# Performance work log

Measured on AMD Instinct MI355X. Metric: run time of the kernel, lower is better.

## Reference

```python
import jax, jax.numpy as jnp
import numpy as np

B, C, H = 16, 256, 32          # batch, in_channels(=out_channels), image_size
HEADS, HS = 8, 32              # heads = out_channels // head_size
D = HEADS * HS                 # head_dim = 256
N = H * H                      # tokens = 1024
EPS = 1e-5


def _rel_indices(h, w):
    # Faithful port of RelativeAttention2d.get_indices
    y = np.arange(h)
    x = np.arange(w)
    y1, x1, y2, x2 = np.meshgrid(y, x, y, x, indexing='ij')
    idx = (y1 - y2 + h - 1) * (2 * w - 1) + (x1 - x2 + w - 1)
    return jnp.asarray(idx.reshape(-1), dtype=jnp.int32)  # [N*N]


def setup_inputs() -> dict:
    key = jax.random.key(0)
    ks = jax.random.split(key, 10)
    s = 0.02
    return {
        'x': jax.random.normal(ks[0], (B, C, H, H), jnp.float32),
        'ln_g': jnp.ones((C,), jnp.float32),
        'ln_b': jnp.zeros((C,), jnp.float32),
        'wq': jax.random.normal(ks[1], (D, C), jnp.float32) * s,
        'bq': jnp.zeros((D,), jnp.float32),
        'wk': jax.random.normal(ks[2], (D, C), jnp.float32) * s,
        'bk': jnp.zeros((D,), jnp.float32),
        'wv': jax.random.normal(ks[3], (D, C), jnp.float32) * s,
        'bv': jnp.zeros((D,), jnp.float32),
        'wo': jax.random.normal(ks[4], (C, D), jnp.float32) * s,
        'bo': jnp.zeros((C,), jnp.float32),
        'rel_bias': jax.random.normal(ks[5], (HEADS, (2 * H - 1) * (2 * H - 1)), jnp.float32),
        'rel_idx': _rel_indices(H, H),
    }


def reference(x, ln_g, ln_b, wq, bq, wk, bk, wv, bv, wo, bo, rel_bias, rel_idx):
    b = x.shape[0]
    # norm(): LayerNorm over channel axis (dim 1 after the double transpose)
    mu = jnp.mean(x, axis=1, keepdims=True)
    var = jnp.mean((x - mu) ** 2, axis=1, keepdims=True)
    xn = (x - mu) / jnp.sqrt(var + EPS)
    xn = xn * ln_g[None, :, None, None] + ln_b[None, :, None, None]
    # reshape_for_linear: raw reshape [b, C, H, W] -> [b, N, C] (as in torch)
    xr = xn.reshape(b, N, C)
    # projections, then raw view(b, heads, head_size, -1) as in torch
    q = (xr @ wq.T + bq).reshape(b, HEADS, HS, N)
    k = (xr @ wk.T + bk).reshape(b, HEADS, HS, N)
    v = (xr @ wv.T + bv).reshape(b, HEADS, HS, N)
    # dots = k^T q / sqrt(head_dim)   [b, heads, N, N]
    dots = jnp.einsum('bhdn,bhdm->bhnm', k, q) / np.float32(np.sqrt(D))
    # gathered relative position bias  [heads, N, N]
    bias = rel_bias[:, rel_idx].reshape(HEADS, N, N)
    attn = jax.nn.softmax(dots + bias[None], axis=-2)  # non-standard softmax dim
    # out = v @ attn  [b, heads, head_size, N]
    out = jnp.einsum('bhdn,bhnm->bhdm', v, attn)
    out = out.reshape(b, H, H, D)  # raw view as in torch
    out = out @ wo.T + bo          # to_output linear (dropout is identity in eval)
    out = out.reshape(b, C, H, H)  # raw view back to [b, out_channels, H, W]
    return x + out
```

## Files before the change

### kernel.cpp

```cpp
#include <hip/hip_runtime.h>
#include <cstdint>

#define PERB 262144
#define LOG2EF 1.4426950408889634f
#define C1F 0.09016844005556022f

typedef __attribute__((ext_vector_type(8))) short bf16x8;
typedef __attribute__((ext_vector_type(4))) float f32x4;
typedef unsigned short ushort_t;

__device__ __forceinline__ uint16_t f2bf(float f) {
    uint32_t u = __float_as_uint(f);
    u += 0x7fff + ((u >> 16) & 1);
    return (uint16_t)(u >> 16);
}

__device__ __forceinline__ void glds16(const void* g, void* l) {
    __builtin_amdgcn_global_load_lds(
        (const __attribute__((address_space(1))) void*)g,
        (__attribute__((address_space(3))) void*)l, 16, 0, 0);
}

__global__ __launch_bounds__(256) void prep_kernel(
    const float* __restrict__ x, const float* __restrict__ gam,
    const float* __restrict__ bet, ushort_t* __restrict__ X,
    const float* __restrict__ wq, const float* __restrict__ wk,
    const float* __restrict__ wv, const float* __restrict__ wo,
    ushort_t* __restrict__ oq, ushort_t* __restrict__ ok,
    ushort_t* __restrict__ ov, ushort_t* __restrict__ oo,
    const float* __restrict__ rb, float* __restrict__ rb2)
{
    const int blk = blockIdx.x;
    const int tid = threadIdx.x;
    if (blk < 256) {
        const int which = blk >> 6;
        const int idx = ((blk & 63) * 256 + tid) * 4;
        const float* src = which == 0 ? wq : which == 1 ? wk : which == 2 ? wv : wo;
        ushort_t* dst    = which == 0 ? oq : which == 1 ? ok : which == 2 ? ov : oo;
        const float4 v = *(const float4*)&src[idx];
        uint2 p;
        p.x = (uint32_t)f2bf(v.x) | ((uint32_t)f2bf(v.y) << 16);
        p.y = (uint32_t)f2bf(v.z) | ((uint32_t)f2bf(v.w) << 16);
        *(uint2*)&dst[idx] = p;
        return;
    }
    if (blk >= 512) {
        const int h = blk - 512;
        const float* s = rb + h * 3969;
        float* d = rb2 + h * 3969;
        for (int i = tid; i < 3969; i += 256) d[i] = s[i] * LOG2EF;
        return;
    }
    const int lb  = blk - 256;
    const int b   = lb >> 4;
    const int sp0 = (lb & 15) << 6;
    const int v   = tid & 15;
    const int cg  = tid >> 4;
    const int sp  = sp0 + v * 4;
    const float* xb = x + (size_t)b * PERB + sp;

    float4 vals[16];
    float4 s4 = {0.f, 0.f, 0.f, 0.f}, q4 = {0.f, 0.f, 0.f, 0.f};
#pragma unroll
    for (int i = 0; i < 16; ++i) {
        const float4 t = *(const float4*)&xb[(size_t)(cg * 16 + i) * 1024];
        vals[i] = t;
        s4.x += t.x; s4.y += t.y; s4.z += t.z; s4.w += t.w;
        q4.x += t.x * t.x; q4.y += t.y * t.y; q4.z += t.z * t.z; q4.w += t.w * t.w;
    }
    __shared__ float red[2][16][64];
    __shared__ float mr[2][64];
    *(float4*)&red[0][cg][v * 4] = s4;
    *(float4*)&red[1][cg][v * 4] = q4;
    __syncthreads();
    if (tid < 64) {
        float ts = 0.f, tq = 0.f;
#pragma unroll
        for (int g = 0; g < 16; ++g) { ts += red[0][g][tid]; tq += red[1][g][tid]; }
        const float mean = ts * (1.f / 256.f);
        const float var  = tq * (1.f / 256.f) - mean * mean;
        mr[0][tid] = mean;
        mr[1][tid] = rsqrtf(var + 1e-5f);
    }
    __syncthreads();
    const float4 mean4 = *(const float4*)&mr[0][v * 4];
    const float4 rstd4 = *(const float4*)&mr[1][v * 4];

    ushort_t* Xb = X + (size_t)b * PERB + sp;
#pragma unroll
    for (int i = 0; i < 16; ++i) {
        const int c = cg * 16 + i;
        const float g = gam[c], be = bet[c];
        const float4 t = vals[i];
        const float y0 = (t.x - mean4.x) * rstd4.x * g + be;
        const float y1 = (t.y - mean4.y) * rstd4.y * g + be;
        const float y2 = (t.z - mean4.z) * rstd4.z * g + be;
        const float y3 = (t.w - mean4.w) * rstd4.w * g + be;
        uint2 p;
        p.x = (uint32_t)f2bf(y0) | ((uint32_t)f2bf(y1) << 16);
        p.y = (uint32_t)f2bf(y2) | ((uint32_t)f2bf(y3) << 16);
        *(uint2*)&Xb[(size_t)c * 1024] = p;
    }
}

__device__ __forceinline__ void qkv_stage(
    ushort_t* Sb, const ushort_t* __restrict__ X,
    const ushort_t* __restrict__ wq, const ushort_t* __restrict__ wk,
    const ushort_t* __restrict__ wv,
    int m0, int n0, int k0, int w, int lane)
{
    const int rsub = lane >> 3;
    const int u    = lane & 7;
    const int koct = u ^ rsub;
#pragma unroll
    for (int i = 0; i < 2; ++i) {
        const int rg  = w * 2 + i;
        const int row = rg * 8 + rsub;
        const int go  = k0 + koct * 8;
        ushort_t* db = Sb + rg * 512;
        glds16(&X [(size_t)(m0 + row) * 256 + go], db);
        glds16(&wq[(size_t)(n0 + row) * 256 + go], db + 4096);
        glds16(&wk[(size_t)(n0 + row) * 256 + go], db + 8192);
        glds16(&wv[(size_t)(n0 + row) * 256 + go], db + 12288);
    }
}

__device__ __forceinline__ void qkv_compute(
    const ushort_t* Sb, int w, int c, int quad, f32x4 acc[3][4])
{
#pragma unroll
    for (int ks = 0; ks < 2; ++ks) {
        const int kq = ks * 4 + quad;
        const int uo = (kq ^ (c & 7)) * 8;
        bf16x8 af[4];
#pragma unroll
        for (int msub = 0; msub < 4; ++msub)
            af[msub] = *(const bf16x8*)&Sb[(msub * 16 + c) * 64 + uo];
        bf16x8 bw[3];
#pragma unroll
        for (int o3 = 0; o3 < 3; ++o3)
            bw[o3] = *(const bf16x8*)&Sb[(o3 + 1) * 4096 + (w * 16 + c) * 64 + uo];
#pragma unroll
        for (int o3 = 0; o3 < 3; ++o3)
#pragma unroll
            for (int msub = 0; msub < 4; ++msub)
                acc[o3][msub] = __builtin_amdgcn_mfma_f32_16x16x32_bf16(
                    bw[o3], af[msub], acc[o3][msub], 0, 0, 0);
    }
}

__global__ __launch_bounds__(256) void qkv_kernel(
    const ushort_t* __restrict__ X,
    const ushort_t* __restrict__ wq, const float* __restrict__ bq,
    const ushort_t* __restrict__ wk, const float* __restrict__ bk,
    const ushort_t* __restrict__ wv, const float* __restrict__ bv,
    ushort_t* __restrict__ Q, ushort_t* __restrict__ K, ushort_t* __restrict__ V)
{
    __shared__ __align__(16) ushort_t SB0[4][4096];
    __shared__ __align__(16) ushort_t SB1[4][4096];

    const int blk = blockIdx.x;
    const int m0  = (blk >> 2) << 6;
    const int n0  = (blk & 3) << 6;
    const int tid = threadIdx.x;
    const int w    = tid >> 6;
    const int lane = tid & 63;
    const int quad = lane >> 4;
    const int c    = lane & 15;

    f32x4 acc[3][4];
#pragma unroll
    for (int o3 = 0; o3 < 3; ++o3)
#pragma unroll
        for (int i = 0; i < 4; ++i) acc[o3][i] = (f32x4){0.f, 0.f, 0.f, 0.f};

    qkv_stage(&SB0[0][0], X, wq, wk, wv, m0, n0, 0, w, lane);
    __syncthreads();
#pragma unroll
    for (int kc = 0; kc < 4; ++kc) {
        if (kc < 3) {
            if ((kc & 1) == 0)
                qkv_stage(&SB1[0][0], X, wq, wk, wv, m0, n0, (kc + 1) << 6, w, lane);
            else
                qkv_stage(&SB0[0][0], X, wq, wk, wv, m0, n0, (kc + 1) << 6, w, lane);
        }
        if ((kc & 1) == 0) qkv_compute(&SB0[0][0], w, c, quad, acc);
        else               qkv_compute(&SB1[0][0], w, c, quad, acc);
        __syncthreads();
    }

    const int n = n0 + w * 16 + quad * 4;
    const float4 bq4 = *(const float4*)&bq[n];
    const float4 bk4 = *(const float4*)&bk[n];
    const float4 bv4 = *(const float4*)&bv[n];
    ushort_t* outs[3] = {Q, K, V};
    const float4 bias[3] = {bq4, bk4, bv4};
#pragma unroll
    for (int msub = 0; msub < 4; ++msub) {
        const size_t m = (size_t)(m0 + msub * 16 + c);
#pragma unroll
        for (int o3 = 0; o3 < 3; ++o3) {
            const f32x4 a = acc[o3][msub];
            uint2 p;
            p.x = (uint32_t)f2bf(a[0] + bias[o3].x) | ((uint32_t)f2bf(a[1] + bias[o3].y) << 16);
            p.y = (uint32_t)f2bf(a[2] + bias[o3].z) | ((uint32_t)f2bf(a[3] + bias[o3].w) << 16);
            *(uint2*)&outs[o3][m * 256 + n] = p;
        }
    }
}

__global__ __launch_bounds__(256, 4) void attn_kernel(
    const ushort_t* __restrict__ Q, const ushort_t* __restrict__ K,
    const ushort_t* __restrict__ V, const float* __restrict__ relb2,
    ushort_t* __restrict__ O)
{
    __shared__ __align__(16) unsigned char smem[32768];
    char* Pb = (char*)smem;
    char* Kl = (char*)(smem + 16384);
    char* Vl = (char*)(smem + 24576);

    const int blk = blockIdx.x;
    const int bh  = blk & 127;
    const int mt  = blk >> 7;
    const int b   = bh >> 3;
    const int h   = bh & 7;
    const int m0  = mt << 7;
    const int tid = threadIdx.x;
    const int w    = tid >> 6;
    const int lane = tid & 63;
    const int quad = lane >> 4;
    const int c    = lane & 15;

    const size_t base = (size_t)b * PERB + (size_t)h * 32768;
    const ushort_t* Qg = Q + base;
    const ushort_t* Kg = K + base;
    const ushort_t* Vg = V + base;
    const float* rbh = relb2 + h * 3969;

    const int knn = tid & 63, ksg = tid >> 6;
    const int vs  = tid >> 3, vng = tid & 7;
    const int kWr = ksg * 1024 + knn * 16;
    const int vWr = vs * 128 + ((vng ^ (vs & 7)) << 4);
    const int c7  = c & 7;

    uint32_t kpre[8]; bf16x8 vpre;
#pragma unroll
    for (int j = 0; j < 8; ++j) kpre[j] = Kg[(size_t)(ksg * 8 + j) * 1024 + knn];
    vpre = *(const bf16x8*)&Vg[(size_t)vs * 1024 + vng * 8];

    {
        const int mm = tid & 127;
        const int sg = tid >> 7;
        union { bf16x8 v; uint16_t u[8]; } g0, g1;
#pragma unroll
        for (int j = 0; j < 8; ++j)
            g0.u[j] = Qg[(size_t)(sg * 16 + j) * 1024 + m0 + mm];
#pragma unroll
        for (int j = 0; j < 8; ++j)
            g1.u[j] = Qg[(size_t)(sg * 16 + 8 + j) * 1024 + m0 + mm];
        *(bf16x8*)(Pb + (sg * 2 + 0) * 2048 + mm * 16) = g0.v;
        *(bf16x8*)(Pb + (sg * 2 + 1) * 2048 + mm * 16) = g1.v;
    }
    {
        uint4 kp;
        kp.x = kpre[0] | (kpre[1] << 16);
        kp.y = kpre[2] | (kpre[3] << 16);
        kp.z = kpre[4] | (kpre[5] << 16);
        kp.w = kpre[6] | (kpre[7] << 16);
        *(uint4*)(Kl + kWr) = kp;
        *(bf16x8*)(Vl + vWr) = vpre;
    }
    __syncthreads();

    bf16x8 qfrag[2];
#pragma unroll
    for (int mi = 0; mi < 2; ++mi)
        qfrag[mi] = *(const bf16x8*)(Pb + quad * 2048 + (((w * 2 + mi) * 16 + c)) * 16);
    __syncthreads();

    int moff[2];
#pragma unroll
    for (int mi = 0; mi < 2; ++mi) {
        const int m = m0 + (w * 2 + mi) * 16 + c;
        moff[mi] = 1984 - (m >> 5) * 63 - (m & 31);
    }
    const int rowb0 = ((w * 2 + 0) * 16 + c) * 128;
    const int rowb1 = ((w * 2 + 1) * 16 + c) * 128;

    f32x4 oacc[2][2], dacc[2];
#pragma unroll
    for (int i = 0; i < 2; ++i) {
        dacc[i] = (f32x4){0.f, 0.f, 0.f, 0.f};
#pragma unroll
        for (int j = 0; j < 2; ++j) oacc[i][j] = (f32x4){0.f, 0.f, 0.f, 0.f};
    }
    bf16x8 onesf;
#pragma unroll
    for (int j = 0; j < 8; ++j) onesf[j] = (short)0x3F80;

#pragma unroll
    for (int j = 0; j < 8; ++j) kpre[j] = Kg[(size_t)(ksg * 8 + j) * 1024 + 64 + knn];
    vpre = *(const bf16x8*)&Vg[(size_t)vs * 1024 + 64 + vng * 8];

    for (int ch = 0; ch < 16; ++ch) {
        const int n0c = ch << 6;
        const int cb  = ch & 1;
        const char* Kc = Kl + (cb << 12);
        const char* Vc = Vl + (cb << 12);

        bf16x8 kf[4];
#pragma unroll
        for (int nsub = 0; nsub < 4; ++nsub)
            kf[nsub] = *(const bf16x8*)(Kc + quad * 1024 + (nsub * 16 + c) * 16);
        f32x4 sacc[2][4];
#pragma unroll
        for (int mi = 0; mi < 2; ++mi)
#pragma unroll
            for (int nsub = 0; nsub < 4; ++nsub) {
                const f32x4 z = {0.f, 0.f, 0.f, 0.f};
                sacc[mi][nsub] = __builtin_amdgcn_mfma_f32_16x16x32_bf16(
                    kf[nsub], qfrag[mi], z, 0, 0, 0);
            }

#pragma unroll
        for (int mi = 0; mi < 2; ++mi) {
            const int rowb = mi ? rowb1 : rowb0;
#pragma unroll
            for (int nsub = 0; nsub < 4; ++nsub) {
                const int nbase = n0c + nsub * 16 + quad * 4;
                const int nidx0 = (nbase >> 5) * 63 + (nbase & 31);
                const float* bp = rbh + nidx0 + moff[mi];
                float p[4];
#pragma unroll
                for (int r = 0; r < 4; ++r)
                    p[r] = __builtin_amdgcn_exp2f(fmaf(sacc[mi][nsub][r], C1F, bp[r]));
                uint2 pk;
                pk.x = __builtin_amdgcn_perm(__float_as_uint(p[1]), __float_as_uint(p[0]), 0x07060302u);
                pk.y = __builtin_amdgcn_perm(__float_as_uint(p[3]), __float_as_uint(p[2]), 0x07060302u);
                const int u = (2 * nsub + (quad >> 1)) ^ c7;
                *(uint2*)(Pb + rowb + u * 16 + ((quad & 1) << 3)) = pk;
            }
        }

#pragma unroll
        for (int kstep = 0; kstep < 2; ++kstep) {
            const int u = ((kstep * 4 + quad) ^ c7) << 4;
            const bf16x8 vf0 = *(const bf16x8*)(Vc + c * 128 + u);
            const bf16x8 vf1 = *(const bf16x8*)(Vc + (16 + c) * 128 + u);
#pragma unroll
            for (int mi = 0; mi < 2; ++mi) {
                const bf16x8 pf = *(const bf16x8*)(Pb + (mi ? rowb1 : rowb0) + u);
                oacc[0][mi] = __builtin_amdgcn_mfma_f32_16x16x32_bf16(vf0, pf, oacc[0][mi], 0, 0, 0);
                oacc[1][mi] = __builtin_amdgcn_mfma_f32_16x16x32_bf16(vf1, pf, oacc[1][mi], 0, 0, 0);
                dacc[mi]    = __builtin_amdgcn_mfma_f32_16x16x32_bf16(onesf, pf, dacc[mi], 0, 0, 0);
            }
        }

        if (ch < 15) {
            const int nb = (cb ^ 1) << 12;
            uint4 kp;
            kp.x = kpre[0] | (kpre[1] << 16);
            kp.y = kpre[2] | (kpre[3] << 16);
            kp.z = kpre[4] | (kpre[5] << 16);
            kp.w = kpre[6] | (kpre[7] << 16);
            *(uint4*)(Kl + nb + kWr) = kp;
            *(bf16x8*)(Vl + nb + vWr) = vpre;
            if (ch < 14) {
                const int n0n = (ch + 2) << 6;
#pragma unroll
                for (int j = 0; j < 8; ++j)
                    kpre[j] = Kg[(size_t)(ksg * 8 + j) * 1024 + n0n + knn];
                vpre = *(const bf16x8*)&Vg[(size_t)vs * 1024 + n0n + vng * 8];
            }
        }
        __syncthreads();
    }

    ushort_t* Ob = O + base;
#pragma unroll
    for (int mi = 0; mi < 2; ++mi) {
        const float inv = 1.0f / dacc[mi][0];
        const int m = m0 + (w * 2 + mi) * 16 + c;
#pragma unroll
        for (int ssub = 0; ssub < 2; ++ssub)
#pragma unroll
            for (int r = 0; r < 4; ++r)
                Ob[(size_t)(ssub * 16 + quad * 4 + r) * 1024 + m] = f2bf(oacc[ssub][mi][r] * inv);
    }
}

__device__ __forceinline__ void oproj_stage(
    ushort_t* Sb, const ushort_t* __restrict__ A, const ushort_t* __restrict__ wo,
    int m0, int n0, int k0, int w, int lane)
{
    const int rsub = lane >> 3;
    const int u    = lane & 7;
    const int koct = u ^ rsub;
#pragma unroll
    for (int i = 0; i < 2; ++i) {
        const int rg  = w * 2 + i;
        const int row = rg * 8 + rsub;
        const int go  = k0 + koct * 8;
        ushort_t* db = Sb + rg * 512;
        glds16(&A [(size_t)(m0 + row) * 256 + go], db);
        glds16(&wo[(size_t)(n0 + row) * 256 + go], db + 4096);
    }
}

__device__ __forceinline__ void oproj_compute(
    const ushort_t* Sb, int w, int c, int quad, f32x4 acc[4])
{
#pragma unroll
    for (int ks = 0; ks < 2; ++ks) {
        const int kq = ks * 4 + quad;
        const int uo = (kq ^ (c & 7)) * 8;
        const bf16x8 bw = *(const bf16x8*)&Sb[4096 + (w * 16 + c) * 64 + uo];
#pragma unroll
        for (int msub = 0; msub < 4; ++msub) {
            const bf16x8 af = *(const bf16x8*)&Sb[(msub * 16 + c) * 64 + uo];
            acc[msub] = __builtin_amdgcn_mfma_f32_16x16x32_bf16(bw, af, acc[msub], 0, 0, 0);
        }
    }
}

__global__ __launch_bounds__(256, 4) void oproj_kernel(
    const ushort_t* __restrict__ A, const ushort_t* __restrict__ wo,
    const float* __restrict__ bo, const float* __restrict__ x,
    float* __restrict__ out)
{
    __shared__ __align__(16) ushort_t SA0[2][4096];
    __shared__ __align__(16) ushort_t SA1[2][4096];

    const int blk = blockIdx.x;
    const int m0  = (blk >> 2) << 6;
    const int n0  = (blk & 3) << 6;
    const int tid = threadIdx.x;
    const int w    = tid >> 6;
    const int lane = tid & 63;
    const int quad = lane >> 4;
    const int c    = lane & 15;

    f32x4 acc[4];
#pragma unroll
    for (int i = 0; i < 4; ++i) acc[i] = (f32x4){0.f, 0.f, 0.f, 0.f};

    oproj_stage(&SA0[0][0], A, wo, m0, n0, 0, w, lane);
    __syncthreads();
#pragma unroll
    for (int kc = 0; kc < 4; ++kc) {
        if (kc < 3) {
            if ((kc & 1) == 0)
                oproj_stage(&SA1[0][0], A, wo, m0, n0, (kc + 1) << 6, w, lane);
            else
                oproj_stage(&SA0[0][0], A, wo, m0, n0, (kc + 1) << 6, w, lane);
        }
        if ((kc & 1) == 0) oproj_compute(&SA0[0][0], w, c, quad, acc);
        else               oproj_compute(&SA1[0][0], w, c, quad, acc);
        __syncthreads();
    }

    const int n = n0 + w * 16 + quad * 4;
    const float4 bo4 = *(const float4*)&bo[n];
#pragma unroll
    for (int msub = 0; msub < 4; ++msub) {
        const size_t g = (size_t)(m0 + msub * 16 + c) * 256 + n;
        const float4 r = *(const float4*)&x[g];
        float4 t;
        t.x = acc[msub][0] + bo4.x + r.x;
        t.y = acc[msub][1] + bo4.y + r.y;
        t.z = acc[msub][2] + bo4.z + r.z;
        t.w = acc[msub][3] + bo4.w + r.w;
        *(float4*)&out[g] = t;
    }
}

extern "C" void kernel_launch(void* const* d_in, const int* in_sizes, int n_in,
                              void* d_out, int out_size, void* d_ws, size_t ws_size,
                              hipStream_t stream)
{
    (void)in_sizes; (void)n_in; (void)out_size; (void)ws_size;
    const float* x   = (const float*)d_in[0];
    const float* lng = (const float*)d_in[1];
    const float* lnb = (const float*)d_in[2];
    const float* wq  = (const float*)d_in[3];
    const float* bq  = (const float*)d_in[4];
    const float* wk  = (const float*)d_in[5];
    const float* bk  = (const float*)d_in[6];
    const float* wv  = (const float*)d_in[7];
    const float* bv  = (const float*)d_in[8];
    const float* wo  = (const float*)d_in[9];
    const float* bo  = (const float*)d_in[10];
    const float* rb  = (const float*)d_in[11];

    ushort_t* ws = (ushort_t*)d_ws;
    ushort_t* Xbf = ws;
    ushort_t* Qbf = ws + 1 * 4194304;
    ushort_t* Kbf = ws + 2 * 4194304;
    ushort_t* Vbf = ws + 3 * 4194304;
    ushort_t* Obf = ws + 4 * 4194304;
    ushort_t* Wqb = ws + 5 * 4194304;
    ushort_t* Wkb = Wqb + 65536;
    ushort_t* Wvb = Wkb + 65536;
    ushort_t* Wob = Wvb + 65536;
    float* rb2 = (float*)(Wob + 65536);
    float* out = (float*)d_out;

    hipLaunchKernelGGL(prep_kernel,  dim3(520),  dim3(256), 0, stream,
                       x, lng, lnb, Xbf, wq, wk, wv, wo, Wqb, Wkb, Wvb, Wob, rb, rb2);
    hipLaunchKernelGGL(qkv_kernel,   dim3(1024), dim3(256), 0, stream,
                       Xbf, Wqb, bq, Wkb, bk, Wvb, bv, Qbf, Kbf, Vbf);
    hipLaunchKernelGGL(attn_kernel,  dim3(1024), dim3(256), 0, stream, Qbf, Kbf, Vbf, rb2, Obf);
    hipLaunchKernelGGL(oproj_kernel, dim3(1024), dim3(256), 0, stream, Obf, Wob, bo, x, out);
}
```

Measured before the change: 156.6 us.

## Halve QKV k-chunk to shrink LDS and add MFMA priority hints in attention

```diff
diff --git a/kernel.cpp b/kernel.cpp
--- a/kernel.cpp
+++ b/kernel.cpp
@@ -109,44 +109,34 @@
     const ushort_t* __restrict__ wv,
     int m0, int n0, int k0, int w, int lane)
 {
-    const int rsub = lane >> 3;
-    const int u    = lane & 7;
-    const int koct = u ^ rsub;
-#pragma unroll
-    for (int i = 0; i < 2; ++i) {
-        const int rg  = w * 2 + i;
-        const int row = rg * 8 + rsub;
-        const int go  = k0 + koct * 8;
-        ushort_t* db = Sb + rg * 512;
-        glds16(&X [(size_t)(m0 + row) * 256 + go], db);
-        glds16(&wq[(size_t)(n0 + row) * 256 + go], db + 4096);
-        glds16(&wk[(size_t)(n0 + row) * 256 + go], db + 8192);
-        glds16(&wv[(size_t)(n0 + row) * 256 + go], db + 12288);
-    }
+    const int row = (w << 4) + (lane >> 2);
+    const int su  = (lane & 3) ^ ((lane >> 3) & 3);
+    const int go  = k0 + su * 8;
+    ushort_t* db = Sb + w * 512;
+    glds16(&X [(size_t)(m0 + row) * 256 + go], db);
+    glds16(&wq[(size_t)(n0 + row) * 256 + go], db + 2048);
+    glds16(&wk[(size_t)(n0 + row) * 256 + go], db + 4096);
+    glds16(&wv[(size_t)(n0 + row) * 256 + go], db + 6144);
 }
 
 __device__ __forceinline__ void qkv_compute(
     const ushort_t* Sb, int w, int c, int quad, f32x4 acc[3][4])
 {
-#pragma unroll
-    for (int ks = 0; ks < 2; ++ks) {
-        const int kq = ks * 4 + quad;
-        const int uo = (kq ^ (c & 7)) * 8;
-        bf16x8 af[4];
+    const int uo = (quad ^ ((c >> 1) & 3)) * 8;
+    bf16x8 bw[3];
+#pragma unroll
+    for (int o3 = 0; o3 < 3; ++o3)
+        bw[o3] = *(const bf16x8*)&Sb[2048 + o3 * 2048 + (w * 16 + c) * 32 + uo];
+    bf16x8 af[4];
+#pragma unroll
+    for (int msub = 0; msub < 4; ++msub)
+        af[msub] = *(const bf16x8*)&Sb[(msub * 16 + c) * 32 + uo];
+#pragma unroll
+    for (int o3 = 0; o3 < 3; ++o3)
 #pragma unroll
         for (int msub = 0; msub < 4; ++msub)
-            af[msub] = *(const bf16x8*)&Sb[(msub * 16 + c) * 64 + uo];
-        bf16x8 bw[3];
-#pragma unroll
-        for (int o3 = 0; o3 < 3; ++o3)
-            bw[o3] = *(const bf16x8*)&Sb[(o3 + 1) * 4096 + (w * 16 + c) * 64 + uo];
-#pragma unroll
-        for (int o3 = 0; o3 < 3; ++o3)
-#pragma unroll
-            for (int msub = 0; msub < 4; ++msub)
-                acc[o3][msub] = __builtin_amdgcn_mfma_f32_16x16x32_bf16(
-                    bw[o3], af[msub], acc[o3][msub], 0, 0, 0);
-    }
+            acc[o3][msub] = __builtin_amdgcn_mfma_f32_16x16x32_bf16(
+                bw[o3], af[msub], acc[o3][msub], 0, 0, 0);
 }
 
 __global__ __launch_bounds__(256) void qkv_kernel(
@@ -156,8 +146,8 @@
     const ushort_t* __restrict__ wv, const float* __restrict__ bv,
     ushort_t* __restrict__ Q, ushort_t* __restrict__ K, ushort_t* __restrict__ V)
 {
-    __shared__ __align__(16) ushort_t SB0[4][4096];
-    __shared__ __align__(16) ushort_t SB1[4][4096];
+    __shared__ __align__(16) ushort_t SB0[8192];
+    __shared__ __align__(16) ushort_t SB1[8192];
 
     const int blk = blockIdx.x;
     const int m0  = (blk >> 2) << 6;
@@ -174,18 +164,18 @@
 #pragma unroll
         for (int i = 0; i < 4; ++i) acc[o3][i] = (f32x4){0.f, 0.f, 0.f, 0.f};
 
-    qkv_stage(&SB0[0][0], X, wq, wk, wv, m0, n0, 0, w, lane);
+    qkv_stage(SB0, X, wq, wk, wv, m0, n0, 0, w, lane);
     __syncthreads();
 #pragma unroll
-    for (int kc = 0; kc < 4; ++kc) {
-        if (kc < 3) {
+    for (int kc = 0; kc < 8; ++kc) {
+        if (kc < 7) {
             if ((kc & 1) == 0)
-                qkv_stage(&SB1[0][0], X, wq, wk, wv, m0, n0, (kc + 1) << 6, w, lane);
+                qkv_stage(SB1, X, wq, wk, wv, m0, n0, (kc + 1) << 5, w, lane);
             else
-                qkv_stage(&SB0[0][0], X, wq, wk, wv, m0, n0, (kc + 1) << 6, w, lane);
-        }
-        if ((kc & 1) == 0) qkv_compute(&SB0[0][0], w, c, quad, acc);
-        else               qkv_compute(&SB1[0][0], w, c, quad, acc);
+                qkv_stage(SB0, X, wq, wk, wv, m0, n0, (kc + 1) << 5, w, lane);
+        }
+        if ((kc & 1) == 0) qkv_compute(SB0, w, c, quad, acc);
+        else               qkv_compute(SB1, w, c, quad, acc);
         __syncthreads();
     }
 
@@ -313,6 +303,7 @@
         for (int nsub = 0; nsub < 4; ++nsub)
             kf[nsub] = *(const bf16x8*)(Kc + quad * 1024 + (nsub * 16 + c) * 16);
         f32x4 sacc[2][4];
+        __builtin_amdgcn_s_setprio(1);
 #pragma unroll
         for (int mi = 0; mi < 2; ++mi)
 #pragma unroll
@@ -321,6 +312,7 @@
                 sacc[mi][nsub] = __builtin_amdgcn_mfma_f32_16x16x32_bf16(
                     kf[nsub], qfrag[mi], z, 0, 0, 0);
             }
+        __builtin_amdgcn_s_setprio(0);
 
 #pragma unroll
         for (int mi = 0; mi < 2; ++mi) {
@@ -342,6 +334,7 @@
             }
         }
 
+        __builtin_amdgcn_s_setprio(1);
 #pragma unroll
         for (int kstep = 0; kstep < 2; ++kstep) {
             const int u = ((kstep * 4 + quad) ^ c7) << 4;
@@ -355,6 +348,7 @@
                 dacc[mi]    = __builtin_amdgcn_mfma_f32_16x16x32_bf16(onesf, pf, dacc[mi], 0, 0, 0);
             }
         }
+        __builtin_amdgcn_s_setprio(0);
 
         if (ch < 15) {
             const int nb = (cb ^ 1) << 12;
```

After: 159.4 us. No clear change (+1.8%).
